# Optimization experiments

Hardware: AMD Instinct MI355X
Metric: run time of the kernel (lower is better)

The kernel has to match this reference:

```python
import jax, jax.numpy as jnp
import numpy as np

N_QUBITS = 8
N_CYCLES = 4
N_LAYERS = 2  # log2(8) - 1
B = 65536

CNOT = jnp.array([[1, 0, 0, 0],
                  [0, 1, 0, 0],
                  [0, 0, 0, 1],
                  [0, 0, 1, 0]], dtype=jnp.complex64)


def apply_gate(state, U, wires):
    """Apply a (2^k x 2^k) gate U on the given wires of state (B, 2,2,...,2).
    Wire 0 is the leftmost (most significant) qubit axis."""
    k = len(wires)
    src = [w + 1 for w in wires]
    dst = list(range(1, 1 + k))
    st = jnp.moveaxis(state, src, dst)
    shp = st.shape
    st = st.reshape(shp[0], 2 ** k, -1)
    st = jnp.einsum('ij,bjr->bir', U, st)
    return jnp.moveaxis(st.reshape(shp), dst, src)


def apply_ry(state, q, angles):
    """Batched RY(angle) on qubit q; angles has shape (B,)."""
    st = jnp.moveaxis(state, q + 1, 1)  # (B, 2, rest...)
    c = jnp.cos(0.5 * angles).reshape((-1,) + (1,) * (st.ndim - 2))
    s = jnp.sin(0.5 * angles).reshape((-1,) + (1,) * (st.ndim - 2))
    s0, s1 = st[:, 0], st[:, 1]
    new = jnp.stack([c * s0 - s * s1, s * s0 + c * s1], axis=1)
    return jnp.moveaxis(new, 1, q + 1)


def crx_mat(theta):
    c = (jnp.cos(0.5 * theta) + 0j).astype(jnp.complex64)
    s = (-1j * jnp.sin(0.5 * theta)).astype(jnp.complex64)
    one = jnp.ones((), jnp.complex64)
    zero = jnp.zeros((), jnp.complex64)
    return jnp.stack([
        jnp.stack([one, zero, zero, zero]),
        jnp.stack([zero, one, zero, zero]),
        jnp.stack([zero, zero, c, s]),
        jnp.stack([zero, zero, s, c]),
    ])


def u3_mat(p):
    th, ph, lm = p[0], p[1], p[2]
    ct = (jnp.cos(0.5 * th) + 0j).astype(jnp.complex64)
    st = (jnp.sin(0.5 * th) + 0j).astype(jnp.complex64)
    el = jnp.exp(1j * lm).astype(jnp.complex64)
    ep = jnp.exp(1j * ph).astype(jnp.complex64)
    return jnp.stack([
        jnp.stack([ct, -el * st]),
        jnp.stack([ep * st, ep * el * ct]),
    ])


def expval_z(state, q):
    st = jnp.moveaxis(state, q + 1, 1)
    p = (st.real ** 2 + st.imag ** 2).reshape(st.shape[0], 2, -1).sum(-1)
    return p[:, 0] - p[:, 1]


def _forward(x, crx_theta, u3_params, w1, b1, w2, b2):
    b = x.shape[0]
    # |0...0> initial state, shape (B, 2,2,...,2)
    state = jnp.zeros((b, 2 ** N_QUBITS), jnp.complex64).at[:, 0].set(1.0)
    state = state.reshape((b,) + (2,) * N_QUBITS)
    # encoder: data re-uploading RY angle encoding + CNOT ring, n_cycles times
    for _ in range(N_CYCLES):
        for q in range(N_QUBITS):
            state = apply_ry(state, q, x[:, q])
        for q in range(N_QUBITS):
            state = apply_gate(state, CNOT, [q, (q + 1) % N_QUBITS])
    # QCNN conv/pool layers with shared weights per layer
    active = list(range(N_QUBITS))
    for layer in range(N_LAYERS):
        U = crx_mat(crx_theta[layer])
        for i in range(0, len(active) - 1, 2):
            state = apply_gate(state, U, [active[i], active[i + 1]])
        for i in range(1, len(active) - 1, 2):
            state = apply_gate(state, U, [active[i], active[i + 1]])
        remain = active[1::2]
        # mid-circuit expval in the original is discarded and does not alter state
        V = u3_mat(u3_params[layer])
        for q in remain:
            state = apply_gate(state, V, [q])
        active = remain
    feats = jnp.stack([expval_z(state, q) for q in active], axis=1)  # (B, 2)
    h = jnp.tanh(feats @ w1 + b1)
    return jax.nn.sigmoid(h @ w2 + b2)  # (B, 1)


def setup_inputs() -> dict:
    key = jax.random.key(0)
    ks = jax.random.split(key, 6)
    return {
        'x': jax.random.normal(ks[0], (B, N_QUBITS), jnp.float32),
        'crx_theta': jax.random.normal(ks[1], (N_LAYERS,), jnp.float32),
        'u3_params': jax.random.normal(ks[2], (N_LAYERS, 3), jnp.float32),
        'w1': jax.random.normal(ks[3], (2, 10), jnp.float32) * 0.5,
        'b1': jnp.zeros((10,), jnp.float32),
        'w2': jax.random.normal(ks[4], (10, 1), jnp.float32) * 0.5,
        'b2': jnp.zeros((1,), jnp.float32),
    }


def reference(x, crx_theta, u3_params, w1, b1, w2, b2):
    return _forward(x, crx_theta, u3_params, w1, b1, w2, b2)
```

## Files before the change

kernel.cpp:

```cpp
#include <hip/hip_runtime.h>


#define NQ 8

typedef float v2 __attribute__((ext_vector_type(2)));

__device__ __forceinline__ v2 sp(float x) { return (v2){x, x}; }
__device__ __forceinline__ v2 fma2(v2 a, v2 b, v2 c) { return __builtin_elementwise_fma(a, b, c); }
__device__ __forceinline__ v2 swp(v2 v) { return __builtin_shufflevector(v, v, 1, 0); }

template<int M>
__device__ __forceinline__ float sx(float v) {
    if constexpr (M == 32) return __shfl_xor(v, 32, 64);
    else return __int_as_float(__builtin_amdgcn_ds_swizzle(
                 __float_as_int(v), (M << 10) | 0x1F));
}
template<int M>
__device__ __forceinline__ v2 sx2(v2 v) {
    v2 r; r.x = sx<M>(v.x); r.y = sx<M>(v.y); return r;
}
__device__ __forceinline__ float bperm(int byte_addr, float v) {
    return __int_as_float(__builtin_amdgcn_ds_bpermute(byte_addr, __float_as_int(v)));
}

#define RY_L(q, M) do { \
    v2 oA = sx2<M>(A), oB = sx2<M>(B); \
    A = fma2(sp(c[q]), A, sp(ts[q]) * oA); \
    B = fma2(sp(c[q]), B, sp(ts[q]) * oB); \
} while(0)

#define CNOT_FUSED() do { \
    v2 TA = pb ? B : A; \
    v2 TS = pb ? A : B; \
    A = (v2){ bperm(ba0, TA.x), bperm(ba1, TA.y) }; \
    B = (v2){ bperm(ba0, TS.y), bperm(ba1, TS.x) }; \
} while(0)

#define CRX_LL(CSH, M, cc, sn) do { \
    const bool ct = (l >> (CSH)) & 1; \
    v2 oRa = sx2<M>(Ra), oIa = sx2<M>(Ia), oRb = sx2<M>(Rb), oIb = sx2<M>(Ib); \
    if (ct) { \
        Ra = fma2(sp(cc), Ra, sp(sn)  * oIa); \
        Ia = fma2(sp(cc), Ia, sp(-(sn)) * oRa); \
        Rb = fma2(sp(cc), Rb, sp(sn)  * oIb); \
        Ib = fma2(sp(cc), Ib, sp(-(sn)) * oRb); \
    } \
} while(0)

#define RYC0(M, T) do { \
    v2 oRa = sx2<M>(Ra), oIa = sx2<M>(Ia), oRb = sx2<M>(Rb), oIb = sx2<M>(Ib); \
    Ra = fma2(sp(uct0), Ra, sp(T) * oRa); Ia = fma2(sp(uct0), Ia, sp(T) * oIa); \
    Rb = fma2(sp(uct0), Rb, sp(T) * oRb); Ib = fma2(sp(uct0), Ib, sp(T) * oIb); \
} while(0)

__global__ void qcnn_prep(const float* __restrict__ crx,
                          const float* __restrict__ u3p,
                          float* __restrict__ ws) {
    if (threadIdx.x == 0 && blockIdx.x == 0) {
        float sc0, cc0, sc1, cc1;
        __sincosf(0.5f * crx[0], &sc0, &cc0);
        __sincosf(0.5f * crx[1], &sc1, &cc1);
        ws[0] = cc0; ws[1] = sc0; ws[2] = cc1; ws[3] = sc1;
        float lm0, ph0;
        {
            float th = u3p[0]; ph0 = u3p[1]; lm0 = u3p[2];
            float st_, ct_;
            __sincosf(0.5f * th, &st_, &ct_);
            ws[4] = ct_; ws[5] = st_;
        }
        {
            float th = u3p[3], ph = u3p[4], lm = u3p[5];
            float st_, ct_, sl, cl, sp_, cp, spl, cpl;
            __sincosf(0.5f * th, &st_, &ct_);
            __sincosf(lm, &sl, &cl);
            __sincosf(ph, &sp_, &cp);
            __sincosf(ph + lm, &spl, &cpl);
            ws[8] = ct_;  ws[9] = st_;  ws[10] = cl; ws[11] = sl; ws[12] = cp; ws[13] = sp_;
            ws[14] = -st_ * cl;  ws[15] = -st_ * sl;
            ws[16] =  st_ * cp;  ws[17] =  st_ * sp_;
            ws[18] =  ct_ * cpl; ws[19] =  ct_ * spl;
        }
        for (int k = 0; k < 4; ++k) {
            float kf = (float)k;
            float sA0, cA0, sB0, cB0, sA1, cA1, sB1, cB1;
            __sincosf(kf * lm0,         &sA0, &cA0);
            __sincosf((kf + 1.f) * lm0, &sB0, &cB0);
            __sincosf(kf * ph0,         &sA1, &cA1);
            __sincosf((kf + 1.f) * ph0, &sB1, &cB1);
            float* q = ws + 20 + k * 8;
            q[0] = cA0; q[1] = sA0; q[2] = cB0; q[3] = sB0;
            q[4] = cA1; q[5] = sA1; q[6] = cB1; q[7] = sB1;
        }
    }
}

__global__ __launch_bounds__(256) void qcnn_kernel(
    const float* __restrict__ x,
    const float* __restrict__ ws,
    const float* __restrict__ w1,
    const float* __restrict__ b1,
    const float* __restrict__ w2,
    const float* __restrict__ b2,
    float* __restrict__ out,
    int Btot)
{
    const int gtid = blockIdx.x * blockDim.x + threadIdx.x;
    const int wave = gtid >> 6;
    const int l = threadIdx.x & 63;
    if (wave >= Btot) return;

    const bool pb = __builtin_popcount(l) & 1;
    const int addr0 = (l & 32) | ((l ^ (l >> 1)) & 31);
    const int ba0 = addr0 << 2;
    const int ba1 = ba0 ^ (48 << 2);

    const float4* xv = (const float4*)(x + wave * NQ);
    float4 xa = xv[0], xb = xv[1];
    float c[NQ], s[NQ], ts[6];
    {
        float ang[NQ] = {xa.x, xa.y, xa.z, xa.w, xb.x, xb.y, xb.z, xb.w};
#pragma unroll
        for (int q = 0; q < NQ; ++q) __sincosf(0.5f * ang[q], &s[q], &c[q]);
#pragma unroll
        for (int q = 0; q < 6; ++q) ts[q] = ((l >> (5 - q)) & 1) ? s[q] : -s[q];
    }

    const float crc0 = ws[0], crs0 = ws[1], crc1 = ws[2], crs1 = ws[3];
    const float uct0 = ws[4], ust0 = ws[5];
    const float uct1 = ws[8],  ust1 = ws[9],  cl1 = ws[10], sl1 = ws[11], cp1 = ws[12], sp1 = ws[13];
    const float u01r1 = ws[14], u01i1 = ws[15], u10r1 = ws[16], u10i1 = ws[17], u11r1 = ws[18], u11i1 = ws[19];

    const int ki = ((l >> 4) & 1) + ((l >> 2) & 1) + (l & 1);
    const float4* dtab = (const float4*)(ws + 20 + ki * 8);
    float4 d0 = dtab[0], d1 = dtab[1];
    const v2 CAB_lm = {d0.x, d0.z}, SAB_lm = {d0.y, d0.w};
    const v2 CAB_ph = {d1.x, d1.z}, SAB_ph = {d1.y, d1.w};
    const float tu1 = ((l >> 4) & 1) ? ust0 : -ust0;
    const float tu3 = ((l >> 2) & 1) ? ust0 : -ust0;
    const float tu5 = (l & 1)        ? ust0 : -ust0;

    v2 A, B;
    {
        float pl = (((l >> 5) & 1) ? s[0] : c[0]);
        pl *= (((l >> 4) & 1) ? s[1] : c[1]);
        pl *= (((l >> 3) & 1) ? s[2] : c[2]);
        pl *= (((l >> 2) & 1) ? s[3] : c[3]);
        pl *= (((l >> 1) & 1) ? s[4] : c[4]);
        pl *= ((l & 1) ? s[5] : c[5]);
        v2 cs7 = {c[7], s[7]};
        A = sp(pl * c[6]) * cs7;
        B = sp(pl * s[6]) * cs7;
    }
    CNOT_FUSED();
#pragma unroll
    for (int cyc = 0; cyc < 3; ++cyc) {
        RY_L(0, 32); RY_L(1, 16); RY_L(2, 8); RY_L(3, 4); RY_L(4, 2); RY_L(5, 1);
        {
            v2 nA = fma2(sp(-s[6]), B, sp(c[6]) * A);
            B = fma2(sp(c[6]), B, sp(s[6]) * A);
            A = nA;
        }
        {
            v2 sv = {-s[7], s[7]};
            A = fma2(sp(c[7]), A, sv * swp(A));
            B = fma2(sp(c[7]), B, sv * swp(B));
        }
        CNOT_FUSED();
    }

    v2 Ra = A, Rb = B, Ia = sp(0.f), Ib = sp(0.f);

    {
        const bool ct = (l >> 5) & 1;
        v2 oRa = sx2<16>(Ra), oRb = sx2<16>(Rb);
        if (ct) {
            Ia = sp(-crs0) * oRa; Ra = sp(crc0) * Ra;
            Ib = sp(-crs0) * oRb; Rb = sp(crc0) * Rb;
        }
    }
    CRX_LL(3, 4, crc0, crs0);
    CRX_LL(1, 1, crc0, crs0);
    {
        v2 nRb = fma2(sp(crc0), Rb, sp(crs0) * swp(Ib));
        Ib = fma2(sp(crc0), Ib, sp(-crs0) * swp(Rb));
        Rb = nRb;
    }
    CRX_LL(4, 8, crc0, crs0);
    CRX_LL(2, 2, crc0, crs0);
    {
        if (l & 1) {
            v2 nRa = fma2(sp(crc0), Ra, sp(crs0) * Ib);
            v2 nRb = fma2(sp(crc0), Rb, sp(crs0) * Ia);
            v2 nIa = fma2(sp(crc0), Ia, sp(-crs0) * Rb);
            v2 nIb = fma2(sp(crc0), Ib, sp(-crs0) * Ra);
            Ra = nRa; Rb = nRb; Ia = nIa; Ib = nIb;
        }
    }
    {
        v2 nRa = fma2(CAB_lm, Ra, -SAB_lm * Ia);
        Ia = fma2(CAB_lm, Ia, SAB_lm * Ra); Ra = nRa;
        v2 nRb = fma2(CAB_lm, Rb, -SAB_lm * Ib);
        Ib = fma2(CAB_lm, Ib, SAB_lm * Rb); Rb = nRb;
    }
    RYC0(16, tu1);
    RYC0(4,  tu3);
    RYC0(1,  tu5);
    {
        v2 usv = {-ust0, ust0};
        Ra = fma2(sp(uct0), Ra, usv * swp(Ra));
        Rb = fma2(sp(uct0), Rb, usv * swp(Rb));
        Ia = fma2(sp(uct0), Ia, usv * swp(Ia));
        Ib = fma2(sp(uct0), Ib, usv * swp(Ib));
    }
    {
        v2 nRa = fma2(CAB_ph, Ra, -SAB_ph * Ia);
        Ia = fma2(CAB_ph, Ia, SAB_ph * Ra); Ra = nRa;
        v2 nRb = fma2(CAB_ph, Rb, -SAB_ph * Ib);
        Ib = fma2(CAB_ph, Ib, SAB_ph * Rb); Rb = nRb;
    }

    CRX_LL(4, 4, crc1, crs1);
    {
        if (l & 1) {
            v2 nRa = fma2(sp(crc1), Ra, sp(crs1) * swp(Ia));
            v2 nIa = fma2(sp(crc1), Ia, sp(-crs1) * swp(Ra));
            v2 nRb = fma2(sp(crc1), Rb, sp(crs1) * swp(Ib));
            v2 nIb = fma2(sp(crc1), Ib, sp(-crs1) * swp(Rb));
            Ra = nRa; Ia = nIa; Rb = nRb; Ib = nIb;
        }
    }
    CRX_LL(2, 1, crc1, crs1);
    {
        const bool b = (l >> 2) & 1;
        if (b) {
            v2 nRa = fma2(sp(cl1), Ra, sp(-sl1) * Ia);
            Ia = fma2(sp(cl1), Ia, sp(sl1) * Ra); Ra = nRa;
            v2 nRb = fma2(sp(cl1), Rb, sp(-sl1) * Ib);
            Ib = fma2(sp(cl1), Ib, sp(sl1) * Rb); Rb = nRb;
        }
        const float t = b ? ust1 : -ust1;
        v2 oRa = sx2<4>(Ra), oIa = sx2<4>(Ia), oRb = sx2<4>(Rb), oIb = sx2<4>(Ib);
        Ra = fma2(sp(uct1), Ra, sp(t) * oRa); Ia = fma2(sp(uct1), Ia, sp(t) * oIa);
        Rb = fma2(sp(uct1), Rb, sp(t) * oRb); Ib = fma2(sp(uct1), Ib, sp(t) * oIb);
        if (b) {
            v2 nRa = fma2(sp(cp1), Ra, sp(-sp1) * Ia);
            Ia = fma2(sp(cp1), Ia, sp(sp1) * Ra); Ra = nRa;
            v2 nRb = fma2(sp(cp1), Rb, sp(-sp1) * Ib);
            Ib = fma2(sp(cp1), Ib, sp(sp1) * Rb); Rb = nRb;
        }
    }
    {
        v2 E0 = {uct1, u11r1}, E1 = {u01r1, u10r1};
        v2 E2 = {0.f, -u11i1}, E3 = {-u01i1, -u10i1};
        v2 G2 = {0.f,  u11i1}, G3 = { u01i1,  u10i1};
        v2 sRa = swp(Ra), sIa = swp(Ia), sRb = swp(Rb), sIb = swp(Ib);
        v2 nRa = fma2(E3, sIa, fma2(E2, Ia, fma2(E1, sRa, E0 * Ra)));
        v2 nIa = fma2(G3, sRa, fma2(G2, Ra, fma2(E1, sIa, E0 * Ia)));
        v2 nRb = fma2(E3, sIb, fma2(E2, Ib, fma2(E1, sRb, E0 * Rb)));
        v2 nIb = fma2(G3, sRb, fma2(G2, Rb, fma2(E1, sIb, E0 * Ib)));
        Ra = nRa; Ia = nIa; Rb = nRb; Ib = nIb;
    }

    v2 Na = fma2(Ia, Ia, Ra * Ra);
    v2 Nb = fma2(Ib, Ib, Rb * Rb);
    v2 T = Na + Nb;
    const float sgn = ((l >> 2) & 1) ? -1.0f : 1.0f;
    v2 F = { sgn * (T.x + T.y), T.x - T.y };
    F += sx2<1>(F);
    F += sx2<2>(F);
    F += sx2<4>(F);
    F += sx2<8>(F);
    F += sx2<16>(F);
    F += sx2<32>(F);

    const int k = l & 15;
    float contrib = 0.0f;
    if (k < 10) {
        float z = fmaf(F.x, w1[k], fmaf(F.y, w1[10 + k], b1[k]));
        float e = __expf(2.0f * z);
        float h = (e - 1.0f) / (e + 1.0f);
        contrib = h * w2[k];
    }
    contrib += sx<1>(contrib);
    contrib += sx<2>(contrib);
    contrib += sx<4>(contrib);
    contrib += sx<8>(contrib);
    if (l == 0) {
        float a = contrib + b2[0];
        out[wave] = 1.0f / (1.0f + __expf(-a));
    }
}

extern "C" void kernel_launch(void* const* d_in, const int* in_sizes, int n_in,
                              void* d_out, int out_size, void* d_ws, size_t ws_size,
                              hipStream_t stream) {
    const float* x   = (const float*)d_in[0];
    const float* crx = (const float*)d_in[1];
    const float* u3p = (const float*)d_in[2];
    const float* w1  = (const float*)d_in[3];
    const float* b1  = (const float*)d_in[4];
    const float* w2  = (const float*)d_in[5];
    const float* b2  = (const float*)d_in[6];
    float* out = (float*)d_out;
    float* ws  = (float*)d_ws;

    const int B = in_sizes[0] / NQ;
    hipLaunchKernelGGL(qcnn_prep, dim3(1), dim3(64), 0, stream, crx, u3p, ws);
    const int wavesPerBlock = 256 / 64;
    const int grid = (B + wavesPerBlock - 1) / wavesPerBlock;
    hipLaunchKernelGGL(qcnn_kernel, dim3(grid), dim3(256), 0, stream,
                       x, ws, w1, b1, w2, b2, out, B);
}
```

Before: 128.6 us.

## Process two batch elements per wavefront to raise instruction-level parallelism

Each wavefront now simulates two independent batch samples, interleaving their state updates, swizzles and bpermutes so that two independent dependency chains are in flight. This halves the number of waves launched and amortises the per-wave setup (workspace loads, lane constants, the MLP head) across two samples. The cost is doubled register use per thread, which may lower occupancy. There is also a latent edge case: with an odd batch size the second element would read past the input.

New measurement: 128.7 us. No clear change (+0.1%).

```diff
diff --git a/kernel.cpp b/kernel.cpp
--- a/kernel.cpp
+++ b/kernel.cpp
@@ -23,34 +23,37 @@
     return __int_as_float(__builtin_amdgcn_ds_bpermute(byte_addr, __float_as_int(v)));
 }
 
-#define RY_L(q, M) do { \
-    v2 oA = sx2<M>(A), oB = sx2<M>(B); \
-    A = fma2(sp(c[q]), A, sp(ts[q]) * oA); \
-    B = fma2(sp(c[q]), B, sp(ts[q]) * oB); \
+#define FOR_E _Pragma("unroll") for (int e = 0; e < 2; ++e)
+
+#define RY_L(q, M) do { FOR_E { \
+    v2 oA = sx2<M>(A[e]), oB = sx2<M>(B[e]); \
+    A[e] = fma2(sp(c[e][q]), A[e], sp(ts[e][q]) * oA); \
+    B[e] = fma2(sp(c[e][q]), B[e], sp(ts[e][q]) * oB); } \
 } while(0)
 
-#define CNOT_FUSED() do { \
-    v2 TA = pb ? B : A; \
-    v2 TS = pb ? A : B; \
-    A = (v2){ bperm(ba0, TA.x), bperm(ba1, TA.y) }; \
-    B = (v2){ bperm(ba0, TS.y), bperm(ba1, TS.x) }; \
+#define CNOT_FUSED() do { FOR_E { \
+    v2 TA = pb ? B[e] : A[e]; \
+    v2 TS = pb ? A[e] : B[e]; \
+    A[e] = (v2){ bperm(ba0, TA.x), bperm(ba1, TA.y) }; \
+    B[e] = (v2){ bperm(ba0, TS.y), bperm(ba1, TS.x) }; } \
 } while(0)
 
 #define CRX_LL(CSH, M, cc, sn) do { \
-    const bool ct = (l >> (CSH)) & 1; \
-    v2 oRa = sx2<M>(Ra), oIa = sx2<M>(Ia), oRb = sx2<M>(Rb), oIb = sx2<M>(Ib); \
-    if (ct) { \
-        Ra = fma2(sp(cc), Ra, sp(sn)  * oIa); \
-        Ia = fma2(sp(cc), Ia, sp(-(sn)) * oRa); \
-        Rb = fma2(sp(cc), Rb, sp(sn)  * oIb); \
-        Ib = fma2(sp(cc), Ib, sp(-(sn)) * oRb); \
-    } \
+    const bool ct_ = (l >> (CSH)) & 1; \
+    v2 oRa[2], oIa[2], oRb[2], oIb[2]; \
+    FOR_E { oRa[e]=sx2<M>(Ra[e]); oIa[e]=sx2<M>(Ia[e]); \
+            oRb[e]=sx2<M>(Rb[e]); oIb[e]=sx2<M>(Ib[e]); } \
+    if (ct_) { FOR_E { \
+        Ra[e] = fma2(sp(cc), Ra[e], sp(sn)    * oIa[e]); \
+        Ia[e] = fma2(sp(cc), Ia[e], sp(-(sn)) * oRa[e]); \
+        Rb[e] = fma2(sp(cc), Rb[e], sp(sn)    * oIb[e]); \
+        Ib[e] = fma2(sp(cc), Ib[e], sp(-(sn)) * oRb[e]); } } \
 } while(0)
 
-#define RYC0(M, T) do { \
-    v2 oRa = sx2<M>(Ra), oIa = sx2<M>(Ia), oRb = sx2<M>(Rb), oIb = sx2<M>(Ib); \
-    Ra = fma2(sp(uct0), Ra, sp(T) * oRa); Ia = fma2(sp(uct0), Ia, sp(T) * oIa); \
-    Rb = fma2(sp(uct0), Rb, sp(T) * oRb); Ib = fma2(sp(uct0), Ib, sp(T) * oIb); \
+#define RYC0(M, T) do { FOR_E { \
+    v2 oRa = sx2<M>(Ra[e]), oIa = sx2<M>(Ia[e]), oRb = sx2<M>(Rb[e]), oIb = sx2<M>(Ib[e]); \
+    Ra[e] = fma2(sp(uct0), Ra[e], sp(T) * oRa); Ia[e] = fma2(sp(uct0), Ia[e], sp(T) * oIa); \
+    Rb[e] = fma2(sp(uct0), Rb[e], sp(T) * oRb); Ib[e] = fma2(sp(uct0), Ib[e], sp(T) * oIb); } \
 } while(0)
 
 __global__ void qcnn_prep(const float* __restrict__ crx,
@@ -105,24 +108,37 @@
     int Btot)
 {
     const int gtid = blockIdx.x * blockDim.x + threadIdx.x;
-    const int wave = gtid >> 6;
+    const int w = gtid >> 6;
     const int l = threadIdx.x & 63;
-    if (wave >= Btot) return;
+    const int e0 = w * 2;
+    if (e0 >= Btot) return;
 
     const bool pb = __builtin_popcount(l) & 1;
     const int addr0 = (l & 32) | ((l ^ (l >> 1)) & 31);
     const int ba0 = addr0 << 2;
     const int ba1 = ba0 ^ (48 << 2);
 
-    const float4* xv = (const float4*)(x + wave * NQ);
-    float4 xa = xv[0], xb = xv[1];
-    float c[NQ], s[NQ], ts[6];
-    {
+    float c[2][8], s6[2], s7[2], ts[2][6];
+    v2 A[2], B[2];
+    FOR_E {
+        const float4* xv = (const float4*)(x + (e0 + e) * NQ);
+        float4 xa = xv[0], xb = xv[1];
         float ang[NQ] = {xa.x, xa.y, xa.z, xa.w, xb.x, xb.y, xb.z, xb.w};
+        float sq[NQ];
 #pragma unroll
-        for (int q = 0; q < NQ; ++q) __sincosf(0.5f * ang[q], &s[q], &c[q]);
+        for (int q = 0; q < NQ; ++q) __sincosf(0.5f * ang[q], &sq[q], &c[e][q]);
 #pragma unroll
-        for (int q = 0; q < 6; ++q) ts[q] = ((l >> (5 - q)) & 1) ? s[q] : -s[q];
+        for (int q = 0; q < 6; ++q) ts[e][q] = ((l >> (5 - q)) & 1) ? sq[q] : -sq[q];
+        s6[e] = sq[6]; s7[e] = sq[7];
+        float pl = (((l >> 5) & 1) ? sq[0] : c[e][0]);
+        pl *= (((l >> 4) & 1) ? sq[1] : c[e][1]);
+        pl *= (((l >> 3) & 1) ? sq[2] : c[e][2]);
+        pl *= (((l >> 2) & 1) ? sq[3] : c[e][3]);
+        pl *= (((l >> 1) & 1) ? sq[4] : c[e][4]);
+        pl *= ((l & 1) ? sq[5] : c[e][5]);
+        v2 cs7 = {c[e][7], sq[7]};
+        A[e] = sp(pl * c[e][6]) * cs7;
+        B[e] = sp(pl * sq[6]) * cs7;
     }
 
     const float crc0 = ws[0], crs0 = ws[1], crc1 = ws[2], crs1 = ws[3];
@@ -139,155 +155,155 @@
     const float tu3 = ((l >> 2) & 1) ? ust0 : -ust0;
     const float tu5 = (l & 1)        ? ust0 : -ust0;
 
-    v2 A, B;
-    {
-        float pl = (((l >> 5) & 1) ? s[0] : c[0]);
-        pl *= (((l >> 4) & 1) ? s[1] : c[1]);
-        pl *= (((l >> 3) & 1) ? s[2] : c[2]);
-        pl *= (((l >> 2) & 1) ? s[3] : c[3]);
-        pl *= (((l >> 1) & 1) ? s[4] : c[4]);
-        pl *= ((l & 1) ? s[5] : c[5]);
-        v2 cs7 = {c[7], s[7]};
-        A = sp(pl * c[6]) * cs7;
-        B = sp(pl * s[6]) * cs7;
-    }
     CNOT_FUSED();
 #pragma unroll
     for (int cyc = 0; cyc < 3; ++cyc) {
         RY_L(0, 32); RY_L(1, 16); RY_L(2, 8); RY_L(3, 4); RY_L(4, 2); RY_L(5, 1);
-        {
-            v2 nA = fma2(sp(-s[6]), B, sp(c[6]) * A);
-            B = fma2(sp(c[6]), B, sp(s[6]) * A);
-            A = nA;
-        }
-        {
-            v2 sv = {-s[7], s[7]};
-            A = fma2(sp(c[7]), A, sv * swp(A));
-            B = fma2(sp(c[7]), B, sv * swp(B));
+        FOR_E {
+            v2 nA = fma2(sp(-s6[e]), B[e], sp(c[e][6]) * A[e]);
+            B[e] = fma2(sp(c[e][6]), B[e], sp(s6[e]) * A[e]);
+            A[e] = nA;
+        }
+        FOR_E {
+            v2 sv = {-s7[e], s7[e]};
+            A[e] = fma2(sp(c[e][7]), A[e], sv * swp(A[e]));
+            B[e] = fma2(sp(c[e][7]), B[e], sv * swp(B[e]));
         }
         CNOT_FUSED();
     }
 
-    v2 Ra = A, Rb = B, Ia = sp(0.f), Ib = sp(0.f);
+    v2 Ra[2], Rb[2], Ia[2], Ib[2];
+    FOR_E { Ra[e] = A[e]; Rb[e] = B[e]; Ia[e] = sp(0.f); Ib[e] = sp(0.f); }
 
     {
-        const bool ct = (l >> 5) & 1;
-        v2 oRa = sx2<16>(Ra), oRb = sx2<16>(Rb);
-        if (ct) {
-            Ia = sp(-crs0) * oRa; Ra = sp(crc0) * Ra;
-            Ib = sp(-crs0) * oRb; Rb = sp(crc0) * Rb;
-        }
+        const bool ct_ = (l >> 5) & 1;
+        v2 oRa[2], oRb[2];
+        FOR_E { oRa[e] = sx2<16>(Ra[e]); oRb[e] = sx2<16>(Rb[e]); }
+        if (ct_) { FOR_E {
+            Ia[e] = sp(-crs0) * oRa[e]; Ra[e] = sp(crc0) * Ra[e];
+            Ib[e] = sp(-crs0) * oRb[e]; Rb[e] = sp(crc0) * Rb[e];
+        } }
     }
     CRX_LL(3, 4, crc0, crs0);
     CRX_LL(1, 1, crc0, crs0);
-    {
-        v2 nRb = fma2(sp(crc0), Rb, sp(crs0) * swp(Ib));
-        Ib = fma2(sp(crc0), Ib, sp(-crs0) * swp(Rb));
-        Rb = nRb;
+    FOR_E {
+        v2 nRb = fma2(sp(crc0), Rb[e], sp(crs0) * swp(Ib[e]));
+        Ib[e] = fma2(sp(crc0), Ib[e], sp(-crs0) * swp(Rb[e]));
+        Rb[e] = nRb;
     }
     CRX_LL(4, 8, crc0, crs0);
     CRX_LL(2, 2, crc0, crs0);
-    {
-        if (l & 1) {
-            v2 nRa = fma2(sp(crc0), Ra, sp(crs0) * Ib);
-            v2 nRb = fma2(sp(crc0), Rb, sp(crs0) * Ia);
-            v2 nIa = fma2(sp(crc0), Ia, sp(-crs0) * Rb);
-            v2 nIb = fma2(sp(crc0), Ib, sp(-crs0) * Ra);
-            Ra = nRa; Rb = nRb; Ia = nIa; Ib = nIb;
-        }
-    }
-    {
-        v2 nRa = fma2(CAB_lm, Ra, -SAB_lm * Ia);
-        Ia = fma2(CAB_lm, Ia, SAB_lm * Ra); Ra = nRa;
-        v2 nRb = fma2(CAB_lm, Rb, -SAB_lm * Ib);
-        Ib = fma2(CAB_lm, Ib, SAB_lm * Rb); Rb = nRb;
+    if (l & 1) { FOR_E {
+        v2 nRa = fma2(sp(crc0), Ra[e], sp(crs0) * Ib[e]);
+        v2 nRb = fma2(sp(crc0), Rb[e], sp(crs0) * Ia[e]);
+        v2 nIa = fma2(sp(crc0), Ia[e], sp(-crs0) * Rb[e]);
+        v2 nIb = fma2(sp(crc0), Ib[e], sp(-crs0) * Ra[e]);
+        Ra[e] = nRa; Rb[e] = nRb; Ia[e] = nIa; Ib[e] = nIb;
+    } }
+    FOR_E {
+        v2 nRa = fma2(CAB_lm, Ra[e], -SAB_lm * Ia[e]);
+        Ia[e] = fma2(CAB_lm, Ia[e], SAB_lm * Ra[e]); Ra[e] = nRa;
+        v2 nRb = fma2(CAB_lm, Rb[e], -SAB_lm * Ib[e]);
+        Ib[e] = fma2(CAB_lm, Ib[e], SAB_lm * Rb[e]); Rb[e] = nRb;
     }
     RYC0(16, tu1);
     RYC0(4,  tu3);
     RYC0(1,  tu5);
-    {
+    FOR_E {
         v2 usv = {-ust0, ust0};
-        Ra = fma2(sp(uct0), Ra, usv * swp(Ra));
-        Rb = fma2(sp(uct0), Rb, usv * swp(Rb));
-        Ia = fma2(sp(uct0), Ia, usv * swp(Ia));
-        Ib = fma2(sp(uct0), Ib, usv * swp(Ib));
-    }
-    {
-        v2 nRa = fma2(CAB_ph, Ra, -SAB_ph * Ia);
-        Ia = fma2(CAB_ph, Ia, SAB_ph * Ra); Ra = nRa;
-        v2 nRb = fma2(CAB_ph, Rb, -SAB_ph * Ib);
-        Ib = fma2(CAB_ph, Ib, SAB_ph * Rb); Rb = nRb;
+        Ra[e] = fma2(sp(uct0), Ra[e], usv * swp(Ra[e]));
+        Rb[e] = fma2(sp(uct0), Rb[e], usv * swp(Rb[e]));
+        Ia[e] = fma2(sp(uct0), Ia[e], usv * swp(Ia[e]));
+        Ib[e] = fma2(sp(uct0), Ib[e], usv * swp(Ib[e]));
+    }
+    FOR_E {
+        v2 nRa = fma2(CAB_ph, Ra[e], -SAB_ph * Ia[e]);
+        Ia[e] = fma2(CAB_ph, Ia[e], SAB_ph * Ra[e]); Ra[e] = nRa;
+        v2 nRb = fma2(CAB_ph, Rb[e], -SAB_ph * Ib[e]);
+        Ib[e] = fma2(CAB_ph, Ib[e], SAB_ph * Rb[e]); Rb[e] = nRb;
     }
 
     CRX_LL(4, 4, crc1, crs1);
-    {
-        if (l & 1) {
-            v2 nRa = fma2(sp(crc1), Ra, sp(crs1) * swp(Ia));
-            v2 nIa = fma2(sp(crc1), Ia, sp(-crs1) * swp(Ra));
-            v2 nRb = fma2(sp(crc1), Rb, sp(crs1) * swp(Ib));
-            v2 nIb = fma2(sp(crc1), Ib, sp(-crs1) * swp(Rb));
-            Ra = nRa; Ia = nIa; Rb = nRb; Ib = nIb;
-        }
-    }
+    if (l & 1) { FOR_E {
+        v2 nRa = fma2(sp(crc1), Ra[e], sp(crs1) * swp(Ia[e]));
+        v2 nIa = fma2(sp(crc1), Ia[e], sp(-crs1) * swp(Ra[e]));
+        v2 nRb = fma2(sp(crc1), Rb[e], sp(crs1) * swp(Ib[e]));
+        v2 nIb = fma2(sp(crc1), Ib[e], sp(-crs1) * swp(Rb[e]));
+        Ra[e] = nRa; Ia[e] = nIa; Rb[e] = nRb; Ib[e] = nIb;
+    } }
     CRX_LL(2, 1, crc1, crs1);
     {
         const bool b = (l >> 2) & 1;
-        if (b) {
-            v2 nRa = fma2(sp(cl1), Ra, sp(-sl1) * Ia);
-            Ia = fma2(sp(cl1), Ia, sp(sl1) * Ra); Ra = nRa;
-            v2 nRb = fma2(sp(cl1), Rb, sp(-sl1) * Ib);
-            Ib = fma2(sp(cl1), Ib, sp(sl1) * Rb); Rb = nRb;
-        }
+        if (b) { FOR_E {
+            v2 nRa = fma2(sp(cl1), Ra[e], sp(-sl1) * Ia[e]);
+            Ia[e] = fma2(sp(cl1), Ia[e], sp(sl1) * Ra[e]); Ra[e] = nRa;
+            v2 nRb = fma2(sp(cl1), Rb[e], sp(-sl1) * Ib[e]);
+            Ib[e] = fma2(sp(cl1), Ib[e], sp(sl1) * Rb[e]); Rb[e] = nRb;
+        } }
         const float t = b ? ust1 : -ust1;
-        v2 oRa = sx2<4>(Ra), oIa = sx2<4>(Ia), oRb = sx2<4>(Rb), oIb = sx2<4>(Ib);
-        Ra = fma2(sp(uct1), Ra, sp(t) * oRa); Ia = fma2(sp(uct1), Ia, sp(t) * oIa);
-        Rb = fma2(sp(uct1), Rb, sp(t) * oRb); Ib = fma2(sp(uct1), Ib, sp(t) * oIb);
-        if (b) {
-            v2 nRa = fma2(sp(cp1), Ra, sp(-sp1) * Ia);
-            Ia = fma2(sp(cp1), Ia, sp(sp1) * Ra); Ra = nRa;
-            v2 nRb = fma2(sp(cp1), Rb, sp(-sp1) * Ib);
-            Ib = fma2(sp(cp1), Ib, sp(sp1) * Rb); Rb = nRb;
-        }
+        v2 oRa[2], oIa[2], oRb[2], oIb[2];
+        FOR_E { oRa[e]=sx2<4>(Ra[e]); oIa[e]=sx2<4>(Ia[e]);
+                oRb[e]=sx2<4>(Rb[e]); oIb[e]=sx2<4>(Ib[e]); }
+        FOR_E {
+            Ra[e] = fma2(sp(uct1), Ra[e], sp(t) * oRa[e]);
+            Ia[e] = fma2(sp(uct1), Ia[e], sp(t) * oIa[e]);
+            Rb[e] = fma2(sp(uct1), Rb[e], sp(t) * oRb[e]);
+            Ib[e] = fma2(sp(uct1), Ib[e], sp(t) * oIb[e]);
+        }
+        if (b) { FOR_E {
+            v2 nRa = fma2(sp(cp1), Ra[e], sp(-sp1) * Ia[e]);
+            Ia[e] = fma2(sp(cp1), Ia[e], sp(sp1) * Ra[e]); Ra[e] = nRa;
+            v2 nRb = fma2(sp(cp1), Rb[e], sp(-sp1) * Ib[e]);
+            Ib[e] = fma2(sp(cp1), Ib[e], sp(sp1) * Rb[e]); Rb[e] = nRb;
+        } }
     }
     {
         v2 E0 = {uct1, u11r1}, E1 = {u01r1, u10r1};
         v2 E2 = {0.f, -u11i1}, E3 = {-u01i1, -u10i1};
         v2 G2 = {0.f,  u11i1}, G3 = { u01i1,  u10i1};
-        v2 sRa = swp(Ra), sIa = swp(Ia), sRb = swp(Rb), sIb = swp(Ib);
-        v2 nRa = fma2(E3, sIa, fma2(E2, Ia, fma2(E1, sRa, E0 * Ra)));
-        v2 nIa = fma2(G3, sRa, fma2(G2, Ra, fma2(E1, sIa, E0 * Ia)));
-        v2 nRb = fma2(E3, sIb, fma2(E2, Ib, fma2(E1, sRb, E0 * Rb)));
-        v2 nIb = fma2(G3, sRb, fma2(G2, Rb, fma2(E1, sIb, E0 * Ib)));
-        Ra = nRa; Ia = nIa; Rb = nRb; Ib = nIb;
-    }
-
-    v2 Na = fma2(Ia, Ia, Ra * Ra);
-    v2 Nb = fma2(Ib, Ib, Rb * Rb);
-    v2 T = Na + Nb;
+        FOR_E {
+            v2 sRa = swp(Ra[e]), sIa = swp(Ia[e]), sRb = swp(Rb[e]), sIb = swp(Ib[e]);
+            v2 nRa = fma2(E3, sIa, fma2(E2, Ia[e], fma2(E1, sRa, E0 * Ra[e])));
+            v2 nIa = fma2(G3, sRa, fma2(G2, Ra[e], fma2(E1, sIa, E0 * Ia[e])));
+            v2 nRb = fma2(E3, sIb, fma2(E2, Ib[e], fma2(E1, sRb, E0 * Rb[e])));
+            v2 nIb = fma2(G3, sRb, fma2(G2, Rb[e], fma2(E1, sIb, E0 * Ib[e])));
+            Ra[e] = nRa; Ia[e] = nIa; Rb[e] = nRb; Ib[e] = nIb;
+        }
+    }
+
+    v2 F[2];
     const float sgn = ((l >> 2) & 1) ? -1.0f : 1.0f;
-    v2 F = { sgn * (T.x + T.y), T.x - T.y };
-    F += sx2<1>(F);
-    F += sx2<2>(F);
-    F += sx2<4>(F);
-    F += sx2<8>(F);
-    F += sx2<16>(F);
-    F += sx2<32>(F);
+    FOR_E {
+        v2 Na = fma2(Ia[e], Ia[e], Ra[e] * Ra[e]);
+        v2 Nb = fma2(Ib[e], Ib[e], Rb[e] * Rb[e]);
+        v2 T = Na + Nb;
+        F[e] = (v2){ sgn * (T.x + T.y), T.x - T.y };
+    }
+    FOR_E { F[e] += sx2<1>(F[e]); }
+    FOR_E { F[e] += sx2<2>(F[e]); }
+    FOR_E { F[e] += sx2<4>(F[e]); }
+    FOR_E { F[e] += sx2<8>(F[e]); }
+    FOR_E { F[e] += sx2<16>(F[e]); }
+    FOR_E { F[e] += sx2<32>(F[e]); }
 
     const int k = l & 15;
+    const int row = l >> 4;
+    const float Fx = (row & 1) ? F[1].x : F[0].x;
+    const float Fy = (row & 1) ? F[1].y : F[0].y;
     float contrib = 0.0f;
     if (k < 10) {
-        float z = fmaf(F.x, w1[k], fmaf(F.y, w1[10 + k], b1[k]));
-        float e = __expf(2.0f * z);
-        float h = (e - 1.0f) / (e + 1.0f);
+        float z = fmaf(Fx, w1[k], fmaf(Fy, w1[10 + k], b1[k]));
+        float ex = __expf(2.0f * z);
+        float h = (ex - 1.0f) / (ex + 1.0f);
         contrib = h * w2[k];
     }
     contrib += sx<1>(contrib);
     contrib += sx<2>(contrib);
     contrib += sx<4>(contrib);
     contrib += sx<8>(contrib);
-    if (l == 0) {
+    if (k == 0 && row < 2) {
         float a = contrib + b2[0];
-        out[wave] = 1.0f / (1.0f + __expf(-a));
+        out[e0 + row] = 1.0f / (1.0f + __expf(-a));
     }
 }
 
@@ -306,8 +322,9 @@
 
     const int B = in_sizes[0] / NQ;
     hipLaunchKernelGGL(qcnn_prep, dim3(1), dim3(64), 0, stream, crx, u3p, ws);
+    const int waves = (B + 1) / 2;
     const int wavesPerBlock = 256 / 64;
-    const int grid = (B + wavesPerBlock - 1) / wavesPerBlock;
+    const int grid = (waves + wavesPerBlock - 1) / wavesPerBlock;
     hipLaunchKernelGGL(qcnn_kernel, dim3(grid), dim3(256), 0, stream,
                        x, ws, w1, b1, w2, b2, out, B);
 }
```
